# Kernel optimization log

Measured on AMD Instinct MI355X. Metric: run time of the kernel, lower is better.

## Reference

```python
import jax, jax.numpy as jnp
import numpy as np

B, T, H, K = 128, 1024, 512, 50


def setup_inputs() -> dict:
    key = jax.random.key(0)
    ks = jax.random.split(key, 6)
    hidden = jax.random.normal(ks[0], (B, T, H), dtype=jnp.float32)
    W = jax.random.normal(ks[1], (K, H), dtype=jnp.float32) * (1.0 / np.sqrt(H))
    b = jax.random.normal(ks[2], (K,), dtype=jnp.float32) * 0.01
    transitions = jax.random.normal(ks[3], (K, K), dtype=jnp.float32) * 0.1
    start_transitions = jax.random.normal(ks[4], (K,), dtype=jnp.float32) * 0.1
    stop_transitions = jax.random.normal(ks[5], (K,), dtype=jnp.float32) * 0.1
    return {"hidden": hidden, "W": W, "b": b, "transitions": transitions,
            "start_transitions": start_transitions, "stop_transitions": stop_transitions}


def _viterbi(feats, transitions, start_transitions, stop_transitions):
    # feats: [B, T, K]. Max-plus DP over time with backpointers.
    v0 = feats[:, 0] + start_transitions  # [B, K]

    def step(v, feat_t):
        # scores[b, i, j] = v[b, i] + transitions[i, j]  (from tag i to tag j)
        scores = v[:, :, None] + transitions[None, :, :]  # [B, K, K]
        bp = jnp.argmax(scores, axis=1)                   # [B, K] best prev tag
        v_new = feat_t + jnp.max(scores, axis=1)          # [B, K]
        return v_new, bp

    feats_rest = jnp.swapaxes(feats[:, 1:], 0, 1)  # [T-1, B, K]
    v_final, bps = jax.lax.scan(step, v0, feats_rest)
    v_final = v_final + stop_transitions

    best_score = jnp.max(v_final, axis=1)                    # [B]
    last_tag = jnp.argmax(v_final, axis=1).astype(jnp.int32)  # [B]

    def back(tag, bp):
        prev = jnp.take_along_axis(bp, tag[:, None], axis=1)[:, 0].astype(jnp.int32)
        return prev, prev

    _, tags_rev = jax.lax.scan(back, last_tag, bps, reverse=True)  # [T-1, B]
    tags = jnp.concatenate([jnp.swapaxes(tags_rev, 0, 1), last_tag[:, None]], axis=1)  # [B, T]
    return best_score, tags


def reference(hidden, W, b, transitions, start_transitions, stop_transitions):
    feats = jnp.einsum('bth,kh->btk', hidden, W) + b  # linear projection
    return _viterbi(feats, transitions, start_transitions, stop_transitions)
```

## Files before the change

kernel.cpp:

```cpp
#include <hip/hip_runtime.h>

#define BB 128
#define TT 1024
#define HH 512
#define KK 50

__device__ __forceinline__ float rl_f(float x, int lane) {
    return __int_as_float(__builtin_amdgcn_readlane(__float_as_int(x), lane));
}

#define PIN10(A,B) asm volatile("" : "+v"(A[B+0]),"+v"(A[B+1]),"+v"(A[B+2]), \
    "+v"(A[B+3]),"+v"(A[B+4]),"+v"(A[B+5]),"+v"(A[B+6]),"+v"(A[B+7]), \
    "+v"(A[B+8]),"+v"(A[B+9]))
#define PIN50(A) do { PIN10(A,0); PIN10(A,10); PIN10(A,20); PIN10(A,30); PIN10(A,40); } while (0)

__global__ __launch_bounds__(256, 4) void gemm_feats(
    const float* __restrict__ hidden, const float* __restrict__ W,
    const float* __restrict__ bias, float* __restrict__ feats)
{
    __shared__ float At[32][132];
    __shared__ float Wt[32][68];
    const int tid = threadIdx.x;
    const int ri  = tid & 31;
    const int ki  = tid >> 5;
    const long row0 = (long)blockIdx.x * 128;

    float acc[4][8];
    #pragma unroll
    for (int r = 0; r < 4; ++r)
        #pragma unroll
        for (int k = 0; k < 8; ++k) acc[r][k] = 0.f;

    for (int h0 = 0; h0 < HH; h0 += 32) {
        #pragma unroll
        for (int it = 0; it < 4; ++it) {
            int idx = tid + 256 * it;
            int r = idx >> 3, hq = idx & 7;
            float4 a = *(const float4*)(hidden + (row0 + r) * HH + h0 + hq * 4);
            At[hq*4+0][r] = a.x; At[hq*4+1][r] = a.y;
            At[hq*4+2][r] = a.z; At[hq*4+3][r] = a.w;
        }
        #pragma unroll
        for (int it = 0; it < 2; ++it) {
            int idx = tid + 256 * it;
            int k = idx >> 3, hq = idx & 7;
            float4 w = make_float4(0.f, 0.f, 0.f, 0.f);
            if (k < KK) w = *(const float4*)(W + k * HH + h0 + hq * 4);
            Wt[hq*4+0][k] = w.x; Wt[hq*4+1][k] = w.y;
            Wt[hq*4+2][k] = w.z; Wt[hq*4+3][k] = w.w;
        }
        __syncthreads();
        #pragma unroll
        for (int h = 0; h < 32; ++h) {
            float a[4], w[8];
            *(float4*)a     = *(const float4*)&At[h][ri * 4];
            *(float4*)w     = *(const float4*)&Wt[h][ki * 8];
            *(float4*)(w+4) = *(const float4*)&Wt[h][ki * 8 + 4];
            #pragma unroll
            for (int r = 0; r < 4; ++r)
                #pragma unroll
                for (int k = 0; k < 8; ++k)
                    acc[r][k] += a[r] * w[k];
        }
        __syncthreads();
    }
    #pragma unroll
    for (int r = 0; r < 4; ++r) {
        long row = row0 + ri * 4 + r;
        #pragma unroll
        for (int k = 0; k < 8; ++k) {
            int kg = ki * 8 + k;
            if (kg < KK) feats[row * KK + kg] = acc[r][k] + bias[kg];
        }
    }
}

__global__ __launch_bounds__(64, 1) void viterbi_fwd(
    float* __restrict__ fv, const float* __restrict__ trans,
    const float* __restrict__ startT, const float* __restrict__ stopT,
    float* __restrict__ out_score, int* __restrict__ lastTag)
{
    const int b  = blockIdx.x;
    const int j  = threadIdx.x;
    const int jc = j < KK ? j : KK - 1;

    float tc[KK];
    #pragma unroll
    for (int i = 0; i < KK; ++i) tc[i] = trans[i * KK + jc];
    PIN50(tc);

    float* p = fv + (size_t)b * TT * KK;
    float v  = p[jc] + startT[jc];
    p[jc] = v;
    float f1 = p[KK + jc];
    float f2 = p[2 * KK + jc];
    float f3 = p[3 * KK + jc];

    #pragma unroll 1
    for (int t = 1; t < TT; ++t) {
        float f = f1; f1 = f2; f2 = f3;
        if (t + 3 < TT) f3 = p[(size_t)(t + 3) * KK + jc];

        float x[KK];
        #pragma unroll
        for (int i = 0; i < KK; ++i) x[i] = rl_f(v, i) + tc[i];

        float y[17];
        #pragma unroll
        for (int i = 0; i < 16; ++i)
            y[i] = fmaxf(fmaxf(x[3*i], x[3*i+1]), x[3*i+2]);
        y[16] = fmaxf(x[48], x[49]);
        float z[6];
        #pragma unroll
        for (int i = 0; i < 5; ++i)
            z[i] = fmaxf(fmaxf(y[3*i], y[3*i+1]), y[3*i+2]);
        z[5] = fmaxf(y[15], y[16]);
        float m = fmaxf(fmaxf(fmaxf(z[0], z[1]), z[2]),
                        fmaxf(fmaxf(z[3], z[4]), z[5]));

        v = f + m;
        p[(size_t)t * KK + jc] = v;
    }

    v += stopT[jc];
    float bestv = rl_f(v, 0); int besti = 0;
    #pragma unroll
    for (int i = 1; i < KK; ++i) {
        float xx = rl_f(v, i);
        if (xx > bestv) { bestv = xx; besti = i; }
    }
    if (j == 0) { out_score[b] = bestv; lastTag[b] = besti; }
}

__global__ __launch_bounds__(64, 4) void bt_maps(
    const float* __restrict__ v, const float* __restrict__ trans,
    unsigned char* __restrict__ bp, int* __restrict__ M)
{
    const int b = blockIdx.x, c = blockIdx.y;
    const int j = threadIdx.x;
    const int jc = j < KK ? j : KK - 1;

    float tc[KK];
    #pragma unroll
    for (int i = 0; i < KK; ++i) tc[i] = trans[i * KK + jc];
    PIN50(tc);

    const float* vb = v + (size_t)b * TT * KK;
    const int lo = c * 32;
    const int hi = min(c * 32 + 31, TT - 2);

    int cur = jc;
    float vnext = vb[(size_t)hi * KK + jc];

    #pragma unroll 1
    for (int s = hi; s >= lo; --s) {
        float vl = vnext;
        if (s > lo) vnext = vb[(size_t)(s - 1) * KK + jc];

        float best = rl_f(vl, 0) + tc[0];
        int   bi   = 0;
        #pragma unroll
        for (int i = 1; i < KK; ++i) {
            float cand = rl_f(vl, i) + tc[i];
            bool g = cand > best;
            best = g ? cand : best;
            bi   = g ? i : bi;
        }

        if (j < KK)
            bp[((size_t)s * BB + b) * KK + j] = (unsigned char)bi;

        cur = __shfl(bi, cur, 64);
    }

    if (j < KK) M[(b * 32 + c) * KK + j] = cur;
}

__global__ void bt_emit(const unsigned char* __restrict__ bp,
                        const int* __restrict__ M,
                        const int* __restrict__ lastTag,
                        float* __restrict__ tags)
{
    __shared__ int Ml[32][KK];
    __shared__ int e[33];
    const int b = blockIdx.x, tid = threadIdx.x;

    for (int i = tid; i < 32 * KK; i += 64)
        Ml[i / KK][i % KK] = M[b * 32 * KK + i];
    __syncthreads();

    if (tid == 0) {
        int cur = lastTag[b];
        e[32] = cur;
        for (int c = 31; c >= 0; --c) { cur = Ml[c][cur]; e[c] = cur; }
    }
    __syncthreads();

    if (tid < 32) {
        const int c  = tid;
        const int lo = c * 32;
        const int hi = min(c * 32 + 31, TT - 2);
        int cur = e[c + 1];
        for (int k = hi; k >= lo; --k) {
            cur = bp[((size_t)k * BB + b) * KK + cur];
            tags[(size_t)b * TT + k] = (float)cur;
        }
    }
    if (tid == 32) tags[(size_t)b * TT + (TT - 1)] = (float)lastTag[b];
}

extern "C" void kernel_launch(void* const* d_in, const int* in_sizes, int n_in,
                              void* d_out, int out_size, void* d_ws, size_t ws_size,
                              hipStream_t stream)
{
    const float* hidden = (const float*)d_in[0];
    const float* W      = (const float*)d_in[1];
    const float* bias   = (const float*)d_in[2];
    const float* trans  = (const float*)d_in[3];
    const float* startT = (const float*)d_in[4];
    const float* stopT  = (const float*)d_in[5];

    float* out = (float*)d_out;

    char* ws = (char*)d_ws;
    float*         fv    = (float*)ws;
    unsigned char* bp    = (unsigned char*)(ws + 26214400);
    int*           M     = (int*)(ws + 32761600);
    int*           lastT = (int*)(ws + 33580800);

    gemm_feats<<<dim3((BB * TT) / 128), 256, 0, stream>>>(hidden, W, bias, fv);
    viterbi_fwd<<<dim3(BB), 64, 0, stream>>>(fv, trans, startT, stopT, out, lastT);
    bt_maps<<<dim3(BB, 32), 64, 0, stream>>>(fv, trans, bp, M);
    bt_emit<<<dim3(BB), 64, 0, stream>>>(bp, M, lastT, out + BB);
}
```

Before: 769.5 us.

## Split Viterbi forward max-reduction across four waves per batch with LDS combine

The forward Viterbi kernel now runs four wavefronts per batch row instead of one. Each wave handles 13 of the 50 source tags with readlane+add+max, then the partial maxima are combined through LDS behind a barrier every timestep. Wave 0 prefetches the emission features and passes them to the other waves through an LDS ring. This shortens the serial per-step dependency chain, but adds a workgroup barrier and LDS round-trip on every one of the 1023 steps.

```diff
diff --git a/kernel.cpp b/kernel.cpp
--- a/kernel.cpp
+++ b/kernel.cpp
@@ -13,6 +13,8 @@
     "+v"(A[B+3]),"+v"(A[B+4]),"+v"(A[B+5]),"+v"(A[B+6]),"+v"(A[B+7]), \
     "+v"(A[B+8]),"+v"(A[B+9]))
 #define PIN50(A) do { PIN10(A,0); PIN10(A,10); PIN10(A,20); PIN10(A,30); PIN10(A,40); } while (0)
+#define PIN13(A) do { PIN10(A,0); \
+    asm volatile("" : "+v"(A[10]),"+v"(A[11]),"+v"(A[12])); } while (0)
 
 __global__ __launch_bounds__(256, 4) void gemm_feats(
     const float* __restrict__ hidden, const float* __restrict__ W,
@@ -75,61 +77,95 @@
     }
 }
 
-__global__ __launch_bounds__(64, 1) void viterbi_fwd(
+__global__ __launch_bounds__(256, 1) void viterbi_fwd(
     float* __restrict__ fv, const float* __restrict__ trans,
     const float* __restrict__ startT, const float* __restrict__ stopT,
     float* __restrict__ out_score, int* __restrict__ lastTag)
 {
-    const int b  = blockIdx.x;
-    const int j  = threadIdx.x;
-    const int jc = j < KK ? j : KK - 1;
-
-    float tc[KK];
-    #pragma unroll
-    for (int i = 0; i < KK; ++i) tc[i] = trans[i * KK + jc];
-    PIN50(tc);
+    __shared__ float pmx[2][4][64];
+    __shared__ float fring[8][64];
+
+    const int b   = blockIdx.x;
+    const int tid = threadIdx.x;
+    const int w   = __builtin_amdgcn_readfirstlane(tid >> 6);
+    const int j   = tid & 63;
+    const int jc  = j < KK ? j : KK - 1;
+    const int istart = w * 13;
+
+    float tc[13];
+    int   iq[13];
+    #pragma unroll
+    for (int q = 0; q < 13; ++q) {
+        int i = istart + q; if (i > KK - 1) i = KK - 1;
+        iq[q] = i;
+        tc[q] = trans[i * KK + jc];
+    }
+    PIN13(tc);
 
     float* p = fv + (size_t)b * TT * KK;
-    float v  = p[jc] + startT[jc];
-    p[jc] = v;
-    float f1 = p[KK + jc];
-    float f2 = p[2 * KK + jc];
-    float f3 = p[3 * KK + jc];
+
+    float v = p[jc] + startT[jc];
+    float f1 = 0.f, f2 = 0.f, f3 = 0.f, f4 = 0.f;
+    if (w == 0) {
+        f1 = p[1 * KK + jc];
+        f2 = p[2 * KK + jc];
+        f3 = p[3 * KK + jc];
+        f4 = p[4 * KK + jc];
+        asm volatile("" : "+v"(f1), "+v"(f2), "+v"(f3), "+v"(f4));
+        fring[1][j] = f1;
+    }
+    asm volatile("" : "+v"(v));
+    asm volatile("s_waitcnt lgkmcnt(0)" ::: "memory");
+    __builtin_amdgcn_s_barrier();
+    asm volatile("" ::: "memory");
+    if (w == 0) p[jc] = v;
 
     #pragma unroll 1
     for (int t = 1; t < TT; ++t) {
-        float f = f1; f1 = f2; f2 = f3;
-        if (t + 3 < TT) f3 = p[(size_t)(t + 3) * KK + jc];
-
-        float x[KK];
-        #pragma unroll
-        for (int i = 0; i < KK; ++i) x[i] = rl_f(v, i) + tc[i];
-
-        float y[17];
-        #pragma unroll
-        for (int i = 0; i < 16; ++i)
-            y[i] = fmaxf(fmaxf(x[3*i], x[3*i+1]), x[3*i+2]);
-        y[16] = fmaxf(x[48], x[49]);
-        float z[6];
-        #pragma unroll
-        for (int i = 0; i < 5; ++i)
-            z[i] = fmaxf(fmaxf(y[3*i], y[3*i+1]), y[3*i+2]);
-        z[5] = fmaxf(y[15], y[16]);
-        float m = fmaxf(fmaxf(fmaxf(z[0], z[1]), z[2]),
-                        fmaxf(fmaxf(z[3], z[4]), z[5]));
-
-        v = f + m;
-        p[(size_t)t * KK + jc] = v;
-    }
-
-    v += stopT[jc];
-    float bestv = rl_f(v, 0); int besti = 0;
-    #pragma unroll
-    for (int i = 1; i < KK; ++i) {
-        float xx = rl_f(v, i);
-        if (xx > bestv) { bestv = xx; besti = i; }
-    }
-    if (j == 0) { out_score[b] = bestv; lastTag[b] = besti; }
+        const int s = t & 1;
+
+        float fcur;
+        if (w == 0) {
+            fcur = f1;
+            fring[(t + 1) & 7][j] = f2;
+            float nf = 0.f;
+            if (t + 4 < TT) nf = p[(size_t)(t + 4) * KK + jc];
+            f1 = f2; f2 = f3; f3 = f4; f4 = nf;
+        } else {
+            fcur = fring[t & 7][j];
+        }
+
+        float x[13];
+        #pragma unroll
+        for (int q = 0; q < 13; ++q) x[q] = rl_f(v, iq[q]) + tc[q];
+
+        float y0 = fmaxf(fmaxf(x[0], x[1]),  x[2]);
+        float y1 = fmaxf(fmaxf(x[3], x[4]),  x[5]);
+        float y2 = fmaxf(fmaxf(x[6], x[7]),  x[8]);
+        float y3 = fmaxf(fmaxf(x[9], x[10]), x[11]);
+        float pm = fmaxf(fmaxf(fmaxf(y0, y1), y2), fmaxf(y3, x[12]));
+
+        pmx[s][w][j] = pm;
+        asm volatile("s_waitcnt lgkmcnt(0)" ::: "memory");
+        __builtin_amdgcn_s_barrier();
+        asm volatile("" ::: "memory");
+        float m = fmaxf(fmaxf(pmx[s][0][j], pmx[s][1][j]),
+                        fmaxf(pmx[s][2][j], pmx[s][3][j]));
+
+        v = fcur + m;
+        if (w == 0) p[(size_t)t * KK + jc] = v;
+    }
+
+    if (w == 0) {
+        v += stopT[jc];
+        float bestv = rl_f(v, 0); int besti = 0;
+        #pragma unroll
+        for (int i = 1; i < KK; ++i) {
+            float xx = rl_f(v, i);
+            if (xx > bestv) { bestv = xx; besti = i; }
+        }
+        if (j == 0) { out_score[b] = bestv; lastTag[b] = besti; }
+    }
 }
 
 __global__ __launch_bounds__(64, 4) void bt_maps(
@@ -229,7 +265,7 @@
     int*           lastT = (int*)(ws + 33580800);
 
     gemm_feats<<<dim3((BB * TT) / 128), 256, 0, stream>>>(hidden, W, bias, fv);
-    viterbi_fwd<<<dim3(BB), 64, 0, stream>>>(fv, trans, startT, stopT, out, lastT);
+    viterbi_fwd<<<dim3(BB), 256, 0, stream>>>(fv, trans, startT, stopT, out, lastT);
     bt_maps<<<dim3(BB, 32), 64, 0, stream>>>(fv, trans, bp, M);
     bt_emit<<<dim3(BB), 64, 0, stream>>>(bp, M, lastT, out + BB);
 }
```

Measured after the change: 889.3 us. +15.6%, slower.

## Prune Viterbi max-plus candidates with cross-lane bound and ballot

Applied to the files above, without the earlier changes.

The forward Viterbi step no longer evaluates all 50 predecessor scores per tag. It builds a global lower bound from max_i(v_i + rowmin_i) using a DPP max reduction. A ballot then keeps only predecessors whose v_i + rowmax_i can reach that bound, and the max is taken over just those, reading transition values from LDS. This aims to cut the per-step VALU and readlane work on the serial time dependency chain, at the cost of a data-dependent loop, extra DPP and LDS latency, and less register-resident data. Feature prefetch depth also grows by one step.

```diff
diff --git a/kernel.cpp b/kernel.cpp
--- a/kernel.cpp
+++ b/kernel.cpp
@@ -13,6 +13,13 @@
     "+v"(A[B+3]),"+v"(A[B+4]),"+v"(A[B+5]),"+v"(A[B+6]),"+v"(A[B+7]), \
     "+v"(A[B+8]),"+v"(A[B+9]))
 #define PIN50(A) do { PIN10(A,0); PIN10(A,10); PIN10(A,20); PIN10(A,30); PIN10(A,40); } while (0)
+
+template <int CTRL>
+__device__ __forceinline__ float dppmax(float x) {
+    int xi = __float_as_int(x);
+    int yi = __builtin_amdgcn_update_dpp(xi, xi, CTRL, 0xf, 0xf, false);
+    return fmaxf(x, __int_as_float(yi));
+}
 
 __global__ __launch_bounds__(256, 4) void gemm_feats(
     const float* __restrict__ hidden, const float* __restrict__ W,
@@ -80,14 +87,24 @@
     const float* __restrict__ startT, const float* __restrict__ stopT,
     float* __restrict__ out_score, int* __restrict__ lastTag)
 {
+    __shared__ float Tl[KK][64];
+
     const int b  = blockIdx.x;
     const int j  = threadIdx.x;
     const int jc = j < KK ? j : KK - 1;
 
-    float tc[KK];
-    #pragma unroll
-    for (int i = 0; i < KK; ++i) tc[i] = trans[i * KK + jc];
-    PIN50(tc);
+    if (j < KK) {
+        #pragma unroll
+        for (int i = 0; i < KK; ++i) Tl[i][j] = trans[i * KK + j];
+    }
+    float rmax = -1e30f, rmin = 1e30f;
+    #pragma unroll
+    for (int q = 0; q < KK; ++q) {
+        float tv = trans[jc * KK + q];
+        rmax = fmaxf(rmax, tv);
+        rmin = fminf(rmin, tv);
+    }
+    __syncthreads();
 
     float* p = fv + (size_t)b * TT * KK;
     float v  = p[jc] + startT[jc];
@@ -95,28 +112,42 @@
     float f1 = p[KK + jc];
     float f2 = p[2 * KK + jc];
     float f3 = p[3 * KK + jc];
+    float f4 = p[4 * KK + jc];
+
+    const unsigned long long lanemask = (1ull << KK) - 1;
 
     #pragma unroll 1
     for (int t = 1; t < TT; ++t) {
-        float f = f1; f1 = f2; f2 = f3;
-        if (t + 3 < TT) f3 = p[(size_t)(t + 3) * KK + jc];
-
-        float x[KK];
-        #pragma unroll
-        for (int i = 0; i < KK; ++i) x[i] = rl_f(v, i) + tc[i];
-
-        float y[17];
-        #pragma unroll
-        for (int i = 0; i < 16; ++i)
-            y[i] = fmaxf(fmaxf(x[3*i], x[3*i+1]), x[3*i+2]);
-        y[16] = fmaxf(x[48], x[49]);
-        float z[6];
-        #pragma unroll
-        for (int i = 0; i < 5; ++i)
-            z[i] = fmaxf(fmaxf(y[3*i], y[3*i+1]), y[3*i+2]);
-        z[5] = fmaxf(y[15], y[16]);
-        float m = fmaxf(fmaxf(fmaxf(z[0], z[1]), z[2]),
-                        fmaxf(fmaxf(z[3], z[4]), z[5]));
+        float f = f1; f1 = f2; f2 = f3; f3 = f4;
+        if (t + 4 < TT) f4 = p[(size_t)(t + 4) * KK + jc];
+
+        float r = v + rmin;
+        r = dppmax<0x111>(r);
+        r = dppmax<0x112>(r);
+        r = dppmax<0x114>(r);
+        r = dppmax<0x118>(r);
+        r = dppmax<0x142>(r);
+        r = dppmax<0x143>(r);
+        float lb = rl_f(r, 63);
+
+        unsigned long long mask = __ballot(v + rmax >= lb) & lanemask;
+        if (mask == 0ull) mask = lanemask;
+
+        int i0 = __builtin_ctzll(mask);
+        unsigned long long m2 = mask & (mask - 1);
+        int i1 = m2 ? __builtin_ctzll(m2) : i0;
+        unsigned long long rest = m2 ? (m2 & (m2 - 1)) : 0ull;
+
+        float t0 = Tl[i0][jc];
+        float t1 = Tl[i1][jc];
+        float x0 = rl_f(v, i0) + t0;
+        float x1 = rl_f(v, i1) + t1;
+        float m  = fmaxf(x0, x1);
+
+        while (rest) {
+            int ii = __builtin_ctzll(rest); rest &= rest - 1;
+            m = fmaxf(m, rl_f(v, ii) + Tl[ii][jc]);
+        }
 
         v = f + m;
         p[(size_t)t * KK + jc] = v;
```

New measurement: 770.9 us. No clear change (+0.2%).
